# Kernel tuning notes

Measured on AMD Instinct MI355X. Metric: run time of the kernel, lower is better.

## Reference

```python
import jax, jax.numpy as jnp
import numpy as np

N, E = 20000, 320000
IN_C, HID, OUT_C, HEADS = 512, 32, 40, 8
NEG_SLOPE = 0.2


def setup_inputs() -> dict:
    key = jax.random.key(0)
    ks = jax.random.split(key, 10)
    x = jax.random.normal(ks[0], (N, IN_C), dtype=jnp.float32)
    edge_index = jax.random.randint(ks[1], (2, E), 0, N, dtype=jnp.int64)
    s1 = 1.0 / np.sqrt(IN_C)
    s2 = 1.0 / np.sqrt(HEADS * HID)
    return {
        "x": x,
        "edge_index": edge_index,
        "w1": jax.random.normal(ks[2], (IN_C, HEADS * HID), dtype=jnp.float32) * s1,
        "att_src1": jax.random.normal(ks[3], (HEADS, HID), dtype=jnp.float32) * s2,
        "att_dst1": jax.random.normal(ks[4], (HEADS, HID), dtype=jnp.float32) * s2,
        "b1": jnp.zeros((HEADS * HID,), dtype=jnp.float32),
        "w2": jax.random.normal(ks[5], (HEADS * HID, OUT_C), dtype=jnp.float32) * s2,
        "att_src2": jax.random.normal(ks[6], (1, OUT_C), dtype=jnp.float32) * 0.15,
        "att_dst2": jax.random.normal(ks[7], (1, OUT_C), dtype=jnp.float32) * 0.15,
        "b2": jnp.zeros((OUT_C,), dtype=jnp.float32),
    }


def gat_conv(x, src, dst, w, att_src, att_dst, bias, heads, out_c, concat):
    n = x.shape[0]
    h = (x @ w).reshape(n, heads, out_c)            # [N,H,C]
    a_s = jnp.sum(h * att_src, axis=-1)             # [N,H]
    a_d = jnp.sum(h * att_dst, axis=-1)             # [N,H]
    e = jax.nn.leaky_relu(a_s[src] + a_d[dst], NEG_SLOPE)  # [E,H]
    # segment softmax over destination nodes (self-loops guarantee nonempty)
    m = jax.ops.segment_max(e, dst, num_segments=n)
    e = jnp.exp(e - m[dst])
    z = jax.ops.segment_sum(e, dst, num_segments=n)
    alpha = e / (z[dst] + 1e-16)                    # [E,H]
    msg = alpha[:, :, None] * h[src]                # [E,H,C]
    out = jax.ops.segment_sum(msg, dst, num_segments=n)  # [N,H,C]
    out = out.reshape(n, heads * out_c) if concat else out.mean(axis=1)
    return out + bias


def reference(x, edge_index, w1, att_src1, att_dst1, b1, w2, att_src2, att_dst2, b2):
    n = x.shape[0]
    loops = jnp.arange(n, dtype=edge_index.dtype)
    src = jnp.concatenate([edge_index[0], loops])
    dst = jnp.concatenate([edge_index[1], loops])
    h = gat_conv(x, src, dst, w1, att_src1, att_dst1, b1, HEADS, HID, True)
    h = jax.nn.elu(h)
    out = gat_conv(h, src, dst, w2, att_src2, att_dst2, b2, 1, OUT_C, False)
    return jax.nn.log_softmax(out, axis=1)
```

## Files before the change

### kernel.cpp

```cpp
#include <hip/hip_runtime.h>
#include <hip/hip_bf16.h>
#include <math.h>

#define N_NODES 20000
#define N_EDGES 320000
#define ET (N_EDGES + N_NODES)
#define IN_C 512
#define HEADS 8
#define HID 32
#define HH (HEADS * HID)
#define OUT_C 40
#define NEG_SLOPE 0.2f

typedef __attribute__((ext_vector_type(8))) short short8;
typedef __attribute__((ext_vector_type(4))) float floatx4;

static __device__ __forceinline__ unsigned short f2bf(float f) {
  __hip_bfloat16 h = __float2bfloat16(f);
  return *(unsigned short*)&h;
}
static __device__ __forceinline__ float bf2f_lo(unsigned int u) {
  return __uint_as_float(u << 16);
}
static __device__ __forceinline__ float bf2f_hi(unsigned int u) {
  return __uint_as_float(u & 0xFFFF0000u);
}

#define WCONV_BLOCKS (IN_C * HH / 256)
#define W2CONV_BLOCKS (HH * OUT_C / 256)
#define COUNT_BLOCKS ((ET + 255) / 256)
__global__ __launch_bounds__(256) void prep_kernel(
    const float* __restrict__ w1, const float* __restrict__ w2,
    const int* __restrict__ ei, unsigned short* __restrict__ wbT,
    unsigned short* __restrict__ w2bT, int* __restrict__ deg) {
  if (blockIdx.x < WCONV_BLOCKS) {
    int j = blockIdx.x * 256 + threadIdx.x;
    int k = j >> 8, n = j & 255;
    wbT[(size_t)n * IN_C + k] = f2bf(w1[j]);
  } else if (blockIdx.x < WCONV_BLOCKS + W2CONV_BLOCKS) {
    int j = (blockIdx.x - WCONV_BLOCKS) * 256 + threadIdx.x;
    int k = j / OUT_C, oc = j % OUT_C;
    w2bT[oc * HH + k] = f2bf(w2[j]);
  } else {
    int e = (blockIdx.x - WCONV_BLOCKS - W2CONV_BLOCKS) * 256 + threadIdx.x;
    if (e < ET) {
      int dst = (e < N_EDGES) ? ei[N_EDGES + e] : (e - N_EDGES);
      atomicAdd(&deg[dst], 1);
    }
  }
}

#define BM 64
#define BN 128
#define BK 32
#define APAD 40
#define GY ((N_NODES + BM - 1) / BM)
#define GEMM_BLOCKS (2 * GY)
__global__ __launch_bounds__(256) void gemm1_kernel(
    const float* __restrict__ X, const unsigned short* __restrict__ BT,
    const float* __restrict__ bias, unsigned short* __restrict__ C,
    const int* __restrict__ deg, int* __restrict__ offs, int* __restrict__ cursor) {
  if (blockIdx.x >= GEMM_BLOCKS) {
    __shared__ int wsum[4];
    int t = threadIdx.x;
    int4 buf[20];
    int s = 0;
    if (t < 250) {
      const int4* dp = (const int4*)deg + t * 20;
#pragma unroll
      for (int i = 0; i < 20; i++) {
        buf[i] = dp[i];
        s += buf[i].x + buf[i].y + buf[i].z + buf[i].w;
      }
    }
    int lane = t & 63, w = t >> 6;
    int inc = s;
    for (int o = 1; o < 64; o <<= 1) {
      int u = __shfl_up(inc, o, 64);
      if (lane >= o) inc += u;
    }
    if (lane == 63) wsum[w] = inc;
    __syncthreads();
    int waveOff = 0;
    for (int i = 0; i < w; i++) waveOff += wsum[i];
    int running = waveOff + inc - s;
    if (t < 250) {
      int base = t * 80;
#pragma unroll
      for (int i = 0; i < 20; i++) {
        int4 v = buf[i];
        int4 o;
        o.x = running;
        o.y = o.x + v.x;
        o.z = o.y + v.y;
        o.w = o.z + v.z;
        running = o.w + v.w;
        *(int4*)(offs + base + i * 4) = o;
        *(int4*)(cursor + base + i * 4) = o;
      }
    }
    if (t == 0) offs[N_NODES] = ET;
    return;
  }
  __shared__ unsigned short As[BM][APAD];
  __shared__ unsigned short Bs[BN][APAD];
  const int tid = threadIdx.x;
  const int lane = tid & 63, wave = tid >> 6;
  const int wm = (wave & 1) * 32;
  const int wn = (wave >> 1) * 64;
  const int r16 = lane & 15, q = lane >> 4;
  const int bx = blockIdx.x & 1, by = blockIdx.x >> 1;
  const int rowBase = by * BM;
  const int colBase = bx * BN;
  floatx4 acc[2][4] = {};

  for (int k0 = 0; k0 < IN_C; k0 += BK) {
    {
      int row = tid >> 2, kc = (tid & 3) * 8;
      int arow = rowBase + row;
      float4 v0 = make_float4(0.f, 0.f, 0.f, 0.f), v1 = v0;
      if (arow < N_NODES) {
        const float* p = X + (size_t)arow * IN_C + k0 + kc;
        v0 = *(const float4*)p;
        v1 = *(const float4*)(p + 4);
      }
      unsigned short tmp[8] = {f2bf(v0.x), f2bf(v0.y), f2bf(v0.z), f2bf(v0.w),
                               f2bf(v1.x), f2bf(v1.y), f2bf(v1.z), f2bf(v1.w)};
      *(float4*)&As[row][kc] = *(const float4*)tmp;
    }
#pragma unroll
    for (int i = 0; i < 2; i++) {
      int c = tid + i * 256;
      int row = c >> 2, kc = (c & 3) * 8;
      float4 v = *(const float4*)(BT + (size_t)(colBase + row) * IN_C + k0 + kc);
      *(float4*)&Bs[row][kc] = v;
    }
    __syncthreads();
    short8 afrag[2], bfrag[4];
#pragma unroll
    for (int mt = 0; mt < 2; mt++)
      afrag[mt] = *(const short8*)&As[wm + mt * 16 + r16][q * 8];
#pragma unroll
    for (int nt = 0; nt < 4; nt++)
      bfrag[nt] = *(const short8*)&Bs[wn + nt * 16 + r16][q * 8];
#pragma unroll
    for (int mt = 0; mt < 2; mt++)
#pragma unroll
      for (int nt = 0; nt < 4; nt++)
        acc[mt][nt] = __builtin_amdgcn_mfma_f32_16x16x32_bf16(
            afrag[mt], bfrag[nt], acc[mt][nt], 0, 0, 0);
    __syncthreads();
  }
#pragma unroll
  for (int mt = 0; mt < 2; mt++) {
#pragma unroll
    for (int nt = 0; nt < 4; nt++) {
      int col = colBase + wn + nt * 16 + r16;
      float bb = bias[col];
#pragma unroll
      for (int r = 0; r < 4; r++) {
        int row = rowBase + wm + mt * 16 + q * 4 + r;
        if (row < N_NODES) C[(size_t)row * HH + col] = f2bf(acc[mt][nt][r] + bb);
      }
    }
  }
}

#define FILL_BLOCKS ((ET + 255) / 256)
#define ATTN1_BLOCKS (N_NODES / 4)
__global__ __launch_bounds__(256) void fill_attn1_kernel(
    const int* __restrict__ ei, int* __restrict__ cursor, int* __restrict__ csr,
    const unsigned short* __restrict__ h1b, const float* __restrict__ asrc,
    const float* __restrict__ adst, float* __restrict__ as1, float* __restrict__ ad1) {
  if (blockIdx.x < FILL_BLOCKS) {
    int e = blockIdx.x * 256 + threadIdx.x;
    if (e >= ET) return;
    int src, dst;
    if (e < N_EDGES) { src = ei[e]; dst = ei[N_EDGES + e]; }
    else { src = e - N_EDGES; dst = src; }
    int pos = atomicAdd(&cursor[dst], 1);
    csr[pos] = src;
  } else {
    int wave = threadIdx.x >> 6, lane = threadIdx.x & 63;
    int n = (blockIdx.x - FILL_BLOCKS) * 4 + wave;
    int c4 = lane * 4;
    uint2 raw = *(const uint2*)(h1b + (size_t)n * HH + c4);
    float h0 = bf2f_lo(raw.x), h1 = bf2f_hi(raw.x);
    float h2 = bf2f_lo(raw.y), h3 = bf2f_hi(raw.y);
    float4 sa = *(const float4*)(asrc + c4);
    float4 sd = *(const float4*)(adst + c4);
    float ps = h0 * sa.x + h1 * sa.y + h2 * sa.z + h3 * sa.w;
    float pd = h0 * sd.x + h1 * sd.y + h2 * sd.z + h3 * sd.w;
#pragma unroll
    for (int o = 4; o > 0; o >>= 1) {
      ps += __shfl_down(ps, o, 8);
      pd += __shfl_down(pd, o, 8);
    }
    if ((lane & 7) == 0) {
      as1[n * HEADS + (lane >> 3)] = ps;
      ad1[n * HEADS + (lane >> 3)] = pd;
    }
  }
}

#define W2ROW 260
#define HROW 260
__global__ __launch_bounds__(256) void layer1_fused_kernel(
    const unsigned short* __restrict__ h1b, const float* __restrict__ as1,
    const float* __restrict__ ad1, const int* __restrict__ offs,
    const int* __restrict__ csr, const float* __restrict__ b1,
    const unsigned short* __restrict__ w2bT, const float* __restrict__ b2,
    const float* __restrict__ asrc2, const float* __restrict__ adst2,
    float* __restrict__ h3, float* __restrict__ as2, float* __restrict__ ad2) {
  __shared__ unsigned short w2s[OUT_C * W2ROW];
  __shared__ float hrow[4][HROW];
  const int tid = threadIdx.x;
#pragma unroll
  for (int i = 0; i < 10; i++) {
    int c = tid + i * 256;
    int row = c >> 6, off = c & 63;
    *(uint2*)&w2s[row * W2ROW + off * 4] = *(const uint2*)(w2bT + row * HH + off * 4);
  }

  int wave = tid >> 6, lane = tid & 63;
  int n = blockIdx.x * 4 + wave;
  int half = lane >> 5;
  int sl = lane & 31;
  int c8 = sl * 8;
  int head = sl >> 2;
  int beg = offs[n], end = offs[n + 1];
  float ad = ad1[n * HEADS + head];
  float acc[8] = {};
  float l = 0.f;
#pragma unroll 2
  for (int k = beg + half; k < end; k += 2) {
    int src = csr[k];
    float e = as1[src * HEADS + head] + ad;
    e = (e > 0.f) ? e : NEG_SLOPE * e;
    float p = __expf(e);
    l += p;
    uint4 raw = *(const uint4*)(h1b + (size_t)src * HH + c8);
    acc[0] = fmaf(p, bf2f_lo(raw.x), acc[0]);
    acc[1] = fmaf(p, bf2f_hi(raw.x), acc[1]);
    acc[2] = fmaf(p, bf2f_lo(raw.y), acc[2]);
    acc[3] = fmaf(p, bf2f_hi(raw.y), acc[3]);
    acc[4] = fmaf(p, bf2f_lo(raw.z), acc[4]);
    acc[5] = fmaf(p, bf2f_hi(raw.z), acc[5]);
    acc[6] = fmaf(p, bf2f_lo(raw.w), acc[6]);
    acc[7] = fmaf(p, bf2f_hi(raw.w), acc[7]);
  }
#pragma unroll
  for (int j = 0; j < 8; j++) acc[j] += __shfl_xor(acc[j], 32, 64);
  l += __shfl_xor(l, 32, 64);
  if (half == 0) {
    float li = 1.f / (l + 1e-16f);
    float4 b0 = *(const float4*)(b1 + c8);
    float4 b4 = *(const float4*)(b1 + c8 + 4);
    float v[8];
    v[0] = acc[0] * li + b0.x; v[1] = acc[1] * li + b0.y;
    v[2] = acc[2] * li + b0.z; v[3] = acc[3] * li + b0.w;
    v[4] = acc[4] * li + b4.x; v[5] = acc[5] * li + b4.y;
    v[6] = acc[6] * li + b4.z; v[7] = acc[7] * li + b4.w;
#pragma unroll
    for (int j = 0; j < 8; j++) v[j] = (v[j] > 0.f) ? v[j] : expm1f(v[j]);
    *(float4*)&hrow[wave][c8] = make_float4(v[0], v[1], v[2], v[3]);
    *(float4*)&hrow[wave][c8 + 4] = make_float4(v[4], v[5], v[6], v[7]);
  }
  __syncthreads();

  float val = 0.f, ps = 0.f, pd = 0.f;
  if (lane < OUT_C) {
    float hacc = 0.f;
#pragma unroll 8
    for (int g = 0; g < HH / 4; g++) {
      float4 hv = *(const float4*)&hrow[wave][g * 4];
      uint2 wv = *(const uint2*)&w2s[lane * W2ROW + g * 4];
      hacc += hv.x * bf2f_lo(wv.x) + hv.y * bf2f_hi(wv.x)
            + hv.z * bf2f_lo(wv.y) + hv.w * bf2f_hi(wv.y);
    }
    val = hacc + b2[lane];
    h3[(size_t)n * OUT_C + lane] = val;
    ps = val * asrc2[lane];
    pd = val * adst2[lane];
  }
#pragma unroll
  for (int o = 32; o > 0; o >>= 1) {
    ps += __shfl_down(ps, o, 64);
    pd += __shfl_down(pd, o, 64);
  }
  if (lane == 0) { as2[n] = ps; ad2[n] = pd; }
}

__global__ __launch_bounds__(256) void agg2_kernel(
    const float* __restrict__ h3, const float* __restrict__ as2,
    const float* __restrict__ ad2, const int* __restrict__ offs,
    const int* __restrict__ csr, const float* __restrict__ b2,
    float* __restrict__ out) {
  int n = blockIdx.x * 4 + (threadIdx.x >> 6);
  int t = threadIdx.x & 63;
  bool act = (t < OUT_C);
  int beg = offs[n], end = offs[n + 1];
  float ad = ad2[n];
  float l = 0.f, acc = 0.f;
#pragma unroll 2
  for (int k = beg; k < end; k++) {
    int src = csr[k];
    float e = as2[src] + ad;
    e = (e > 0.f) ? e : NEG_SLOPE * e;
    float p = __expf(e);
    l += p;
    float hv = act ? h3[(size_t)src * OUT_C + t] : 0.f;
    acc = fmaf(p, hv, acc);
  }
  float v = acc / (l + 1e-16f) + (act ? b2[t] : 0.f);
  float x = act ? v : -INFINITY;
  float mx = x;
  for (int o = 32; o > 0; o >>= 1) mx = fmaxf(mx, __shfl_down(mx, o, 64));
  mx = __shfl(mx, 0, 64);
  float ex = act ? __expf(v - mx) : 0.f;
  float s = ex;
  for (int o = 32; o > 0; o >>= 1) s += __shfl_down(s, o, 64);
  s = __shfl(s, 0, 64);
  if (act) out[(size_t)n * OUT_C + t] = v - mx - logf(s);
}

extern "C" void kernel_launch(void* const* d_in, const int* in_sizes, int n_in,
                              void* d_out, int out_size, void* d_ws, size_t ws_size,
                              hipStream_t stream) {
  const float* x     = (const float*)d_in[0];
  const int*   ei    = (const int*)d_in[1];
  const float* w1    = (const float*)d_in[2];
  const float* asrc1 = (const float*)d_in[3];
  const float* adst1 = (const float*)d_in[4];
  const float* b1    = (const float*)d_in[5];
  const float* w2    = (const float*)d_in[6];
  const float* asrc2 = (const float*)d_in[7];
  const float* adst2 = (const float*)d_in[8];
  const float* b2    = (const float*)d_in[9];
  float* out = (float*)d_out;

  float* fw = (float*)d_ws;
  float* as1   = fw;  fw += (size_t)N_NODES * HEADS;
  float* ad1   = fw;  fw += (size_t)N_NODES * HEADS;
  float* h3    = fw;  fw += (size_t)N_NODES * OUT_C;
  float* as2   = fw;  fw += N_NODES;
  float* ad2   = fw;  fw += N_NODES;
  unsigned short* h1b  = (unsigned short*)fw;  fw += (size_t)N_NODES * HH / 2;
  unsigned short* wbT  = (unsigned short*)fw;  fw += (size_t)IN_C * HH / 2;
  unsigned short* w2bT = (unsigned short*)fw;  fw += (size_t)HH * OUT_C / 2;
  int* deg    = (int*)fw;
  int* offs   = deg + N_NODES;
  int* cursor = offs + N_NODES + 4;
  int* csr    = cursor + N_NODES;

  hipMemsetAsync(deg, 0, N_NODES * sizeof(int), stream);

  prep_kernel<<<WCONV_BLOCKS + W2CONV_BLOCKS + COUNT_BLOCKS, 256, 0, stream>>>(
      w1, w2, ei, wbT, w2bT, deg);
  gemm1_kernel<<<GEMM_BLOCKS + 1, 256, 0, stream>>>(x, wbT, b1, h1b, deg, offs, cursor);
  fill_attn1_kernel<<<FILL_BLOCKS + ATTN1_BLOCKS, 256, 0, stream>>>(
      ei, cursor, csr, h1b, asrc1, adst1, as1, ad1);
  layer1_fused_kernel<<<N_NODES / 4, 256, 0, stream>>>(
      h1b, as1, ad1, offs, csr, b1, w2bT, b2, asrc2, adst2, h3, as2, ad2);
  agg2_kernel<<<N_NODES / 4, 256, 0, stream>>>(h3, as2, ad2, offs, csr, b2, out);
}
```

Baseline: 232.8 us.

## Batch 16 nodes per block and compute layer-2 projection with bf16 MFMA

The fused layer-1 aggregation kernel now handles 16 nodes per block, with each wave aggregating 4 nodes in turn. It stores the ELU outputs as bf16 in shared memory and computes the 256x40 projection with 16x16x32 bf16 MFMA instructions, keeping W2 fragments in registers. This removes the per-block staging of W2 into shared memory and the scalar per-lane dot products, and cuts the block count by four. In exchange it rounds the hidden activations to bf16 before the second matmul, which slightly reduces precision. The aggregation within a wave is also now serialized over its 4 nodes.

```diff
diff --git a/kernel.cpp b/kernel.cpp
--- a/kernel.cpp
+++ b/kernel.cpp
@@ -203,8 +203,8 @@
   }
 }
 
-#define W2ROW 260
-#define HROW 260
+#define NPB 16
+#define H2ROW 264
 __global__ __launch_bounds__(256) void layer1_fused_kernel(
     const unsigned short* __restrict__ h1b, const float* __restrict__ as1,
     const float* __restrict__ ad1, const int* __restrict__ offs,
@@ -212,83 +212,111 @@
     const unsigned short* __restrict__ w2bT, const float* __restrict__ b2,
     const float* __restrict__ asrc2, const float* __restrict__ adst2,
     float* __restrict__ h3, float* __restrict__ as2, float* __restrict__ ad2) {
-  __shared__ unsigned short w2s[OUT_C * W2ROW];
-  __shared__ float hrow[4][HROW];
+  __shared__ __align__(16) unsigned short h2s[NPB][H2ROW];
+  __shared__ float psum[3][NPB], pdsum[3][NPB];
   const int tid = threadIdx.x;
-#pragma unroll
-  for (int i = 0; i < 10; i++) {
-    int c = tid + i * 256;
-    int row = c >> 6, off = c & 63;
-    *(uint2*)&w2s[row * W2ROW + off * 4] = *(const uint2*)(w2bT + row * HH + off * 4);
-  }
-
-  int wave = tid >> 6, lane = tid & 63;
-  int n = blockIdx.x * 4 + wave;
-  int half = lane >> 5;
-  int sl = lane & 31;
-  int c8 = sl * 8;
-  int head = sl >> 2;
-  int beg = offs[n], end = offs[n + 1];
-  float ad = ad1[n * HEADS + head];
-  float acc[8] = {};
-  float l = 0.f;
+  const int wave = tid >> 6, lane = tid & 63;
+  const int r16 = lane & 15, q = lane >> 4;
+  const int nodeBase = blockIdx.x * NPB;
+
+  short8 bfrag[8];
+  float sa = 0.f, sd = 0.f, b2c = 0.f;
+  if (wave < 3) {
+    int col = wave * 16 + r16;
+    int colc = (col < OUT_C) ? col : 0;
+#pragma unroll
+    for (int s = 0; s < 8; s++)
+      bfrag[s] = *(const short8*)(w2bT + colc * HH + s * 32 + q * 8);
+    if (col < OUT_C) { sa = asrc2[col]; sd = adst2[col]; b2c = b2[col]; }
+  }
+
+  const int half = lane >> 5, sl = lane & 31;
+  const int c8 = sl * 8, head = sl >> 2;
+  float4 b0 = *(const float4*)(b1 + c8);
+  float4 b4 = *(const float4*)(b1 + c8 + 4);
+  for (int i = 0; i < 4; i++) {
+    int local = wave * 4 + i;
+    int n = nodeBase + local;
+    int beg = offs[n], end = offs[n + 1];
+    float ad = ad1[n * HEADS + head];
+    float acc[8] = {};
+    float l = 0.f;
 #pragma unroll 2
-  for (int k = beg + half; k < end; k += 2) {
-    int src = csr[k];
-    float e = as1[src * HEADS + head] + ad;
-    e = (e > 0.f) ? e : NEG_SLOPE * e;
-    float p = __expf(e);
-    l += p;
-    uint4 raw = *(const uint4*)(h1b + (size_t)src * HH + c8);
-    acc[0] = fmaf(p, bf2f_lo(raw.x), acc[0]);
-    acc[1] = fmaf(p, bf2f_hi(raw.x), acc[1]);
-    acc[2] = fmaf(p, bf2f_lo(raw.y), acc[2]);
-    acc[3] = fmaf(p, bf2f_hi(raw.y), acc[3]);
-    acc[4] = fmaf(p, bf2f_lo(raw.z), acc[4]);
-    acc[5] = fmaf(p, bf2f_hi(raw.z), acc[5]);
-    acc[6] = fmaf(p, bf2f_lo(raw.w), acc[6]);
-    acc[7] = fmaf(p, bf2f_hi(raw.w), acc[7]);
-  }
-#pragma unroll
-  for (int j = 0; j < 8; j++) acc[j] += __shfl_xor(acc[j], 32, 64);
-  l += __shfl_xor(l, 32, 64);
-  if (half == 0) {
-    float li = 1.f / (l + 1e-16f);
-    float4 b0 = *(const float4*)(b1 + c8);
-    float4 b4 = *(const float4*)(b1 + c8 + 4);
-    float v[8];
-    v[0] = acc[0] * li + b0.x; v[1] = acc[1] * li + b0.y;
-    v[2] = acc[2] * li + b0.z; v[3] = acc[3] * li + b0.w;
-    v[4] = acc[4] * li + b4.x; v[5] = acc[5] * li + b4.y;
-    v[6] = acc[6] * li + b4.z; v[7] = acc[7] * li + b4.w;
-#pragma unroll
-    for (int j = 0; j < 8; j++) v[j] = (v[j] > 0.f) ? v[j] : expm1f(v[j]);
-    *(float4*)&hrow[wave][c8] = make_float4(v[0], v[1], v[2], v[3]);
-    *(float4*)&hrow[wave][c8 + 4] = make_float4(v[4], v[5], v[6], v[7]);
+    for (int k = beg + half; k < end; k += 2) {
+      int src = csr[k];
+      float e = as1[src * HEADS + head] + ad;
+      e = (e > 0.f) ? e : NEG_SLOPE * e;
+      float p = __expf(e);
+      l += p;
+      uint4 raw = *(const uint4*)(h1b + ((unsigned)src << 8) + c8);
+      acc[0] = fmaf(p, bf2f_lo(raw.x), acc[0]);
+      acc[1] = fmaf(p, bf2f_hi(raw.x), acc[1]);
+      acc[2] = fmaf(p, bf2f_lo(raw.y), acc[2]);
+      acc[3] = fmaf(p, bf2f_hi(raw.y), acc[3]);
+      acc[4] = fmaf(p, bf2f_lo(raw.z), acc[4]);
+      acc[5] = fmaf(p, bf2f_hi(raw.z), acc[5]);
+      acc[6] = fmaf(p, bf2f_lo(raw.w), acc[6]);
+      acc[7] = fmaf(p, bf2f_hi(raw.w), acc[7]);
+    }
+#pragma unroll
+    for (int j = 0; j < 8; j++) acc[j] += __shfl_xor(acc[j], 32, 64);
+    l += __shfl_xor(l, 32, 64);
+    if (half == 0) {
+      float li = 1.f / (l + 1e-16f);
+      float v[8];
+      v[0] = acc[0] * li + b0.x; v[1] = acc[1] * li + b0.y;
+      v[2] = acc[2] * li + b0.z; v[3] = acc[3] * li + b0.w;
+      v[4] = acc[4] * li + b4.x; v[5] = acc[5] * li + b4.y;
+      v[6] = acc[6] * li + b4.z; v[7] = acc[7] * li + b4.w;
+      unsigned short o8[8];
+#pragma unroll
+      for (int j = 0; j < 8; j++) {
+        float e = (v[j] > 0.f) ? v[j] : expm1f(v[j]);
+        o8[j] = f2bf(e);
+      }
+      *(uint4*)&h2s[local][c8] = *(const uint4*)o8;
+    }
   }
   __syncthreads();
 
-  float val = 0.f, ps = 0.f, pd = 0.f;
-  if (lane < OUT_C) {
-    float hacc = 0.f;
-#pragma unroll 8
-    for (int g = 0; g < HH / 4; g++) {
-      float4 hv = *(const float4*)&hrow[wave][g * 4];
-      uint2 wv = *(const uint2*)&w2s[lane * W2ROW + g * 4];
-      hacc += hv.x * bf2f_lo(wv.x) + hv.y * bf2f_hi(wv.x)
-            + hv.z * bf2f_lo(wv.y) + hv.w * bf2f_hi(wv.y);
-    }
-    val = hacc + b2[lane];
-    h3[(size_t)n * OUT_C + lane] = val;
-    ps = val * asrc2[lane];
-    pd = val * adst2[lane];
-  }
-#pragma unroll
-  for (int o = 32; o > 0; o >>= 1) {
-    ps += __shfl_down(ps, o, 64);
-    pd += __shfl_down(pd, o, 64);
-  }
-  if (lane == 0) { as2[n] = ps; ad2[n] = pd; }
+  if (wave < 3) {
+    floatx4 dacc = {};
+#pragma unroll
+    for (int s = 0; s < 8; s++) {
+      short8 afrag = *(const short8*)&h2s[r16][s * 32 + q * 8];
+      dacc = __builtin_amdgcn_mfma_f32_16x16x32_bf16(afrag, bfrag[s], dacc, 0, 0, 0);
+    }
+    int col = wave * 16 + r16;
+    float psr[4], pdr[4];
+#pragma unroll
+    for (int r = 0; r < 4; r++) {
+      float val = dacc[r] + b2c;
+      if (col < OUT_C)
+        h3[(size_t)(nodeBase + q * 4 + r) * OUT_C + col] = val;
+      psr[r] = val * sa;
+      pdr[r] = val * sd;
+    }
+#pragma unroll
+    for (int o = 8; o > 0; o >>= 1) {
+#pragma unroll
+      for (int r = 0; r < 4; r++) {
+        psr[r] += __shfl_down(psr[r], o, 16);
+        pdr[r] += __shfl_down(pdr[r], o, 16);
+      }
+    }
+    if (r16 == 0) {
+#pragma unroll
+      for (int r = 0; r < 4; r++) {
+        psum[wave][q * 4 + r] = psr[r];
+        pdsum[wave][q * 4 + r] = pdr[r];
+      }
+    }
+  }
+  __syncthreads();
+  if (tid < NPB) {
+    as2[nodeBase + tid] = psum[0][tid] + psum[1][tid] + psum[2][tid];
+    ad2[nodeBase + tid] = pdsum[0][tid] + pdsum[1][tid] + pdsum[2][tid];
+  }
 }
 
 __global__ __launch_bounds__(256) void agg2_kernel(
@@ -360,7 +388,7 @@
   gemm1_kernel<<<GEMM_BLOCKS + 1, 256, 0, stream>>>(x, wbT, b1, h1b, deg, offs, cursor);
   fill_attn1_kernel<<<FILL_BLOCKS + ATTN1_BLOCKS, 256, 0, stream>>>(
       ei, cursor, csr, h1b, asrc1, adst1, as1, ad1);
-  layer1_fused_kernel<<<N_NODES / 4, 256, 0, stream>>>(
+  layer1_fused_kernel<<<N_NODES / NPB, 256, 0, stream>>>(
       h1b, as1, ad1, offs, csr, b1, w2bT, b2, asrc2, adst2, h3, as2, ad2);
   agg2_kernel<<<N_NODES / 4, 256, 0, stream>>>(h3, as2, ad2, offs, csr, b2, out);
 }
```

Result: no change. 235.0 us (+0.9%).
